# Kernel tuning notes

Measured on AMD Instinct MI355X. Metric: run time of the kernel, lower is better.

The kernel has to match this reference:

```python
import jax, jax.numpy as jnp
import numpy as np

# WikiText-103 adaptive softmax config
CUTOFFS = (0, 20000, 40000, 200000, 267735)  # cluster boundaries


def setup_inputs() -> dict:
    key = jax.random.key(0)
    ks = jax.random.split(key, 12)
    N, D = 1024, 1024
    rn = lambda k, shape, std: jax.random.normal(k, shape, jnp.float32) * std
    return {
        "hidden": jax.random.normal(ks[0], (N, D), jnp.float32),
        "target": jax.random.randint(ks[1], (N,), 0, CUTOFFS[-1], jnp.int32),
        "head_w": rn(ks[2], (20000, 1024), 0.02),
        "head_b": jnp.zeros((20000,), jnp.float32),
        "cluster_w": rn(ks[3], (3, 1024), 0.02),
        "cluster_b": jnp.zeros((3,), jnp.float32),
        "proj0": rn(ks[4], (1024, 1024), 0.01),
        "proj1": rn(ks[5], (1024, 256), 0.01),
        "proj2": rn(ks[6], (1024, 64), 0.01),
        "proj3": rn(ks[7], (1024, 16), 0.01),
        "w1": rn(ks[8], (20000, 256), 0.02),
        "b1": jnp.zeros((20000,), jnp.float32),
        "w2": rn(ks[9], (160000, 64), 0.02),
        "b2": jnp.zeros((160000,), jnp.float32),
        "w3": rn(ks[10], (67735, 16), 0.02),
        "b3": jnp.zeros((67735,), jnp.float32),
    }


def _logit(h, w, b, proj):
    # F.linear(F.linear(h, proj.t()), w, b) == (h @ proj) @ w.T + b
    return (h @ proj) @ w.T + b


def reference(hidden, target, head_w, head_b, cluster_w, cluster_b,
              proj0, proj1, proj2, proj3, w1, b1, w2, b2, w3, b3):
    # head: shortlist vocab (20000) + 3 cluster logits -> [N, 20003]
    hw = jnp.concatenate([head_w, cluster_w], axis=0)
    hb = jnp.concatenate([head_b, cluster_b], axis=0)
    head_lp = jax.nn.log_softmax(_logit(hidden, hw, hb, proj0), axis=-1)

    # cluster 0 (shortlist): logprob directly from head
    t0 = jnp.clip(target, 0, CUTOFFS[1] - 1)
    lp = jnp.take_along_axis(head_lp, t0[:, None].astype(jnp.int32), axis=1)[:, 0]

    tails = [(w1, b1, proj1), (w2, b2, proj2), (w3, b3, proj3)]
    for i, (w, b, p) in enumerate(tails, start=1):
        l, r = CUTOFFS[i], CUTOFFS[i + 1]
        mask = (target >= l) & (target < r)
        ti = jnp.clip(target - l, 0, r - l - 1)
        tail_lp = jax.nn.log_softmax(_logit(hidden, w, b, p), axis=-1)  # [N, r-l]
        # note: torch code indexes head_logprob[:, -i] (reversed cluster order quirk)
        lpi = head_lp[:, -i] + jnp.take_along_axis(tail_lp, ti[:, None], axis=1)[:, 0]
        lp = jnp.where(mask, lpi, lp)

    return -lp  # nll per token, keep_order semantics
```

## Files before the change

kernel.cpp:

```cpp
#include <hip/hip_runtime.h>
#include <math.h>

typedef __bf16 bf16;
typedef __bf16 bf16x4 __attribute__((ext_vector_type(4)));
typedef __bf16 bf16x8 __attribute__((ext_vector_type(8)));
typedef float  f32x4  __attribute__((ext_vector_type(4)));

__device__ __forceinline__ f32x4 mfma16x16x32(bf16x8 a, bf16x8 b, f32x4 c) {
  return __builtin_amdgcn_mfma_f32_16x16x32_bf16(a, b, c, 0, 0, 0);
}

__device__ __forceinline__ void async16(const bf16* gp, bf16* lp) {
  __builtin_amdgcn_global_load_lds(
      (const __attribute__((address_space(1))) void*)gp,
      (__attribute__((address_space(3))) void*)lp, 16, 0, 0);
}

__global__ void __launch_bounds__(256) megaconvert_kernel(
    const float* __restrict__ hidden, const float* __restrict__ head_w,
    const float* __restrict__ cluster_w, const float* __restrict__ w1,
    const float* __restrict__ w2, const float* __restrict__ w3,
    bf16* __restrict__ hid_b, bf16* __restrict__ Wh, bf16* __restrict__ W1b,
    bf16* __restrict__ W2b, bf16* __restrict__ W3b) {
  int b = blockIdx.x;
  const float* in; bf16* out; int n4, tot; int w3mode = 0;
  if (b < 1024)       { in = hidden;    out = hid_b; n4 = 262144;  tot = 262144;  }
  else if (b < 21024) { in = head_w;    out = Wh;    n4 = 5120000; tot = 5120000; b -= 1024; }
  else if (b < 21120) { in = cluster_w; out = Wh + (size_t)20000 * 1024; n4 = 768; tot = 24576; b -= 21024; }
  else if (b < 26144) { in = w1;        out = W1b;   n4 = 1280000; tot = 1286144; b -= 21120; }
  else if (b < 36144) { in = w2;        out = W2b;   n4 = 2560000; tot = 2560000; b -= 26144; }
  else                { in = w3;        out = W3b;   n4 = 270940;  tot = 271360;  b -= 36144; w3mode = 1; }
  int i = b * 256 + threadIdx.x;
  if (i >= tot) return;
  bf16x4 z = {(bf16)0.f, (bf16)0.f, (bf16)0.f, (bf16)0.f};
  bf16x4 v = z;
  if (i < n4) {
    float4 f = ((const float4*)in)[i];
    v = (bf16x4){(bf16)f.x, (bf16)f.y, (bf16)f.z, (bf16)f.w};
  }
  if (!w3mode) {
    ((bf16x4*)out)[i] = v;
  } else {
    int row = i >> 2, kq = i & 3;
    *(bf16x4*)&out[(size_t)row * 32 + kq * 4] = v;
    *(bf16x4*)&out[(size_t)row * 32 + 16 + kq * 4] = z;
  }
}

__global__ void __launch_bounds__(256) transpose_all_kernel(
    const float* __restrict__ proj0, const float* __restrict__ proj1,
    const float* __restrict__ proj2, const float* __restrict__ proj3,
    bf16* __restrict__ Pcat) {
  __shared__ float t[32][33];
  int y = blockIdx.y;
  const float* P; bf16* Pt; int dX, cy;
  if (y < 32)      { P = proj0; Pt = Pcat;                        dX = 1024; cy = y; }
  else if (y < 40) { P = proj1; Pt = Pcat + (size_t)1024 * 1024;  dX = 256;  cy = y - 32; }
  else if (y < 42) { P = proj2; Pt = Pcat + (size_t)1280 * 1024;  dX = 64;   cy = y - 40; }
  else             { P = proj3; Pt = Pcat + (size_t)1344 * 1024;  dX = 16;   cy = y - 42; }
  int tx = threadIdx.x & 31, ty = threadIdx.x >> 5;
  int k0 = blockIdx.x * 32, c0 = cy * 32;
#pragma unroll
  for (int s = 0; s < 4; ++s) {
    int k = k0 + ty + s * 8, col = c0 + tx;
    t[ty + s * 8][tx] = (col < dX) ? P[(size_t)k * dX + col] : 0.f;
  }
  __syncthreads();
#pragma unroll
  for (int s = 0; s < 4; ++s) {
    int colo = c0 + ty + s * 8;
    Pt[(size_t)colo * 1024 + k0 + tx] = (bf16)t[tx][ty + s * 8];
  }
}

__global__ void __launch_bounds__(1024) compact_kernel(const int* __restrict__ target,
                                                       int* __restrict__ rowmap,
                                                       int* __restrict__ slotmap,
                                                       int* __restrict__ counts) {
  __shared__ int cnt[3];
  int tid = threadIdx.x;
  if (tid < 3) cnt[tid] = 0;
  for (int i = tid; i < 3 * 1152; i += 1024) rowmap[i] = 0;
  __syncthreads();
  int t = target[tid];
  int c = (t >= 200000) ? 2 : (t >= 40000) ? 1 : (t >= 20000) ? 0 : -1;
  int slot = -1;
  if (c >= 0) {
    slot = atomicAdd(&cnt[c], 1);
    rowmap[c * 1152 + slot] = tid;
  }
  slotmap[tid] = slot;
  __syncthreads();
  if (tid < 3) counts[tid] = cnt[tid];
}

template <int KDIM, bool LSE>
__global__ void __launch_bounds__(256) gemm_kernel(
    const bf16* __restrict__ A, int strideA,
    const int* __restrict__ rmap, const int* __restrict__ cntp,
    const bf16* __restrict__ B,
    const float* __restrict__ bias, const float* __restrict__ bias2,
    int splice, int V, float* __restrict__ part, int nchunk,
    bf16* __restrict__ Out, int strideOut, int dX) {
  constexpr int BK = 64;
  constexpr int KG = 8;
  constexpr int NIT = KDIM / BK;
  __shared__ bf16 Alds[2][128 * BK];
  __shared__ bf16 Blds[2][128 * BK];
  __shared__ float wpart[2][128];

  const int tid = threadIdx.x;
  const int w = tid >> 6, lane = tid & 63;
  const int q = lane >> 4, c = lane & 15;
  const int wr = w >> 1, wc = w & 1;

  int f = blockIdx.x;
  int xr = f & 7, rb = (f >> 3) & 7, cq = f >> 6;
  int chunk = cq * 8 + xr;
  if (chunk >= nchunk) return;
  const int row0 = rb * 128, col0 = chunk * 128;
  if (cntp && row0 >= *cntp) return;

  int arow[4];
#pragma unroll
  for (int i = 0; i < 4; ++i) {
    int g = i * 256 + tid;
    int r = row0 + (g >> 3);
    arow[i] = rmap ? rmap[r] : r;
  }

  auto stage = [&](int kt, int pb) {
    const int k0 = kt * BK;
#pragma unroll
    for (int i = 0; i < 4; ++i) {
      int g = i * 256 + tid;
      int col = g >> 3, j = g & 7;
      int kg = j ^ (col & 7);
      async16(A + (size_t)arow[i] * strideA + k0 + kg * 8,
              &Alds[pb][(size_t)(g & ~63) * 8]);
      async16(B + (size_t)(col0 + col) * KDIM + k0 + kg * 8,
              &Blds[pb][(size_t)(g & ~63) * 8]);
    }
  };

  f32x4 acc[4][4] = {};

  stage(0, 0);
  for (int kt = 0; kt < NIT; ++kt) {
    const int cb = kt & 1;
    if (kt + 1 < NIT) {
      stage(kt + 1, cb ^ 1);
      asm volatile("s_waitcnt vmcnt(8)" ::: "memory");
    } else {
      asm volatile("s_waitcnt vmcnt(0)" ::: "memory");
    }
    __builtin_amdgcn_sched_barrier(0);
    __builtin_amdgcn_s_barrier();
    asm volatile("" ::: "memory");
    __builtin_amdgcn_s_setprio(1);
#pragma unroll
    for (int ks = 0; ks < BK / 32; ++ks) {
      bf16x8 af[4], bfr[4];
#pragma unroll
      for (int rt = 0; rt < 4; ++rt) {
        int rl = wr * 64 + rt * 16 + c;
        int kq = ks * 4 + q;
        int kg = kq ^ (rl & 7);
        af[rt] = *(const bf16x8*)&Alds[cb][((size_t)rl * KG + kg) * 8];
      }
#pragma unroll
      for (int ct = 0; ct < 4; ++ct) {
        int cl = wc * 64 + ct * 16 + c;
        int kq = ks * 4 + q;
        int kg = kq ^ (cl & 7);
        bfr[ct] = *(const bf16x8*)&Blds[cb][((size_t)cl * KG + kg) * 8];
      }
#pragma unroll
      for (int rt = 0; rt < 4; ++rt)
#pragma unroll
        for (int ct = 0; ct < 4; ++ct)
          acc[rt][ct] = mfma16x16x32(af[rt], bfr[ct], acc[rt][ct]);
    }
    __builtin_amdgcn_s_setprio(0);
    asm volatile("" ::: "memory");
    __builtin_amdgcn_s_barrier();
  }

  if (!LSE) {
#pragma unroll
    for (int rt = 0; rt < 4; ++rt)
#pragma unroll
      for (int ct = 0; ct < 4; ++ct)
#pragma unroll
        for (int r = 0; r < 4; ++r) {
          int col = col0 + wc * 64 + ct * 16 + c;
          if (col < dX) {
            int row = row0 + wr * 64 + rt * 16 + q * 4 + r;
            Out[(size_t)row * strideOut + col] = (bf16)acc[rt][ct][r];
          }
        }
    return;
  }

  float bv[4];
#pragma unroll
  for (int ct = 0; ct < 4; ++ct) {
    int colg = col0 + wc * 64 + ct * 16 + c;
    bv[ct] = (colg < V) ? ((colg < splice) ? bias[colg] : bias2[colg - splice]) : -INFINITY;
  }
#pragma unroll
  for (int rt = 0; rt < 4; ++rt) {
#pragma unroll
    for (int r = 0; r < 4; ++r) {
      float s = 0.f;
#pragma unroll
      for (int ct = 0; ct < 4; ++ct) s += __expf(acc[rt][ct][r] + bv[ct]);
#pragma unroll
      for (int off = 1; off <= 8; off <<= 1) s += __shfl_xor(s, off);
      if (c == 0) wpart[wc][wr * 64 + rt * 16 + q * 4 + r] = s;
    }
  }
  __syncthreads();
  if (tid < 128)
    part[(size_t)chunk * 1024 + row0 + tid] = __logf(wpart[0][tid] + wpart[1][tid]);
}

template <int KDIM, int G>
__global__ void __launch_bounds__(256) gemm_lse_wide_kernel(
    const bf16* __restrict__ A, int strideA,
    const int* __restrict__ rmap, const int* __restrict__ cntp,
    const bf16* __restrict__ B, const float* __restrict__ bias,
    int V, float* __restrict__ part, int nchunk) {
  constexpr int BK = KDIM;
  constexpr int KG = BK / 8;
  constexpr int NL = KG / 2;
  __shared__ bf16 Alds[128 * BK];
  __shared__ bf16 Blds[3][128 * BK];
  __shared__ float biasl[G * 128];
  __shared__ float spart[2][128];

  const int tid = threadIdx.x;
  const int w = tid >> 6, lane = tid & 63;
  const int q = lane >> 4, c = lane & 15;
  const int wr = w >> 1, wc = w & 1;

  const int row0 = blockIdx.y * 128;
  if (row0 >= *cntp) return;
  const int chunk0 = blockIdx.x * G;
  const int nc = (nchunk - chunk0 < G) ? (nchunk - chunk0) : G;

  for (int i = tid; i < G * 128; i += 256) {
    int colg = chunk0 * 128 + i;
    biasl[i] = (colg < V) ? bias[colg] : -INFINITY;
  }
#pragma unroll
  for (int i = 0; i < NL; ++i) {
    int g = i * 256 + tid;
    int row = g / KG, j = g % KG;
    int kg = (KG == 8) ? (j ^ (row & 7)) : (j ^ ((row >> 1) & 3));
    int ar = rmap[row0 + row];
    async16(A + (size_t)ar * strideA + kg * 8, &Alds[(size_t)(g & ~63) * 8]);
  }
#pragma unroll
  for (int b = 0; b < 2; ++b) {
    int ck = (b < nc) ? b : nc - 1;
#pragma unroll
    for (int i = 0; i < NL; ++i) {
      int g = i * 256 + tid;
      int col = g / KG, j = g % KG;
      int kg = (KG == 8) ? (j ^ (col & 7)) : (j ^ ((col >> 1) & 3));
      async16(B + (size_t)((chunk0 + ck) * 128 + col) * KDIM + kg * 8,
              &Blds[b][(size_t)(g & ~63) * 8]);
    }
  }
  __syncthreads();

  bf16x8 af[BK / 32][4];
#pragma unroll
  for (int ks = 0; ks < BK / 32; ++ks)
#pragma unroll
    for (int rt = 0; rt < 4; ++rt) {
      int rl = wr * 64 + rt * 16 + c;
      int kq = ks * 4 + q;
      int kg = (KG == 8) ? (kq ^ (rl & 7)) : (kq ^ ((rl >> 1) & 3));
      af[ks][rt] = *(const bf16x8*)&Alds[((size_t)rl * KG + kg) * 8];
    }

  float sums[4][4] = {};
  int ib = 0;

  for (int ci = 0; ci < nc; ++ci) {
    {
      int pre = (ci + 2 < nc) ? ci + 2 : nc - 1;
      bf16* bw = Blds[(ib == 0) ? 2 : ib - 1];
#pragma unroll
      for (int i = 0; i < NL; ++i) {
        int g = i * 256 + tid;
        int col = g / KG, j = g % KG;
        int kg = (KG == 8) ? (j ^ (col & 7)) : (j ^ ((col >> 1) & 3));
        async16(B + (size_t)((chunk0 + pre) * 128 + col) * KDIM + kg * 8,
                &bw[(size_t)(g & ~63) * 8]);
      }
    }

    const bf16* Bl = Blds[ib];
    f32x4 acc[4][4] = {};
#pragma unroll
    for (int ks = 0; ks < BK / 32; ++ks) {
      bf16x8 bfr[4];
#pragma unroll
      for (int ct = 0; ct < 4; ++ct) {
        int cl = wc * 64 + ct * 16 + c;
        int kq = ks * 4 + q;
        int kg = (KG == 8) ? (kq ^ (cl & 7)) : (kq ^ ((cl >> 1) & 3));
        bfr[ct] = *(const bf16x8*)&Bl[((size_t)cl * KG + kg) * 8];
      }
#pragma unroll
      for (int rt = 0; rt < 4; ++rt)
#pragma unroll
        for (int ct = 0; ct < 4; ++ct)
          acc[rt][ct] = mfma16x16x32(af[ks][rt], bfr[ct], acc[rt][ct]);
    }

    float bv[4];
#pragma unroll
    for (int ct = 0; ct < 4; ++ct) bv[ct] = biasl[ci * 128 + wc * 64 + ct * 16 + c];
#pragma unroll
    for (int rt = 0; rt < 4; ++rt)
#pragma unroll
      for (int r = 0; r < 4; ++r) {
#pragma unroll
        for (int ct = 0; ct < 4; ++ct)
          sums[rt][r] += __expf(acc[rt][ct][r] + bv[ct]);
      }

    if constexpr (NL == 4) asm volatile("s_waitcnt vmcnt(4)" ::: "memory");
    else                   asm volatile("s_waitcnt vmcnt(2)" ::: "memory");
    __builtin_amdgcn_sched_barrier(0);
    __builtin_amdgcn_s_barrier();
    ib = (ib == 2) ? 0 : ib + 1;
  }

#pragma unroll
  for (int rt = 0; rt < 4; ++rt)
#pragma unroll
    for (int r = 0; r < 4; ++r) {
      float s = sums[rt][r];
#pragma unroll
      for (int off = 1; off <= 8; off <<= 1) s += __shfl_xor(s, off);
      if (c == 0) spart[wc][wr * 64 + rt * 16 + q * 4 + r] = s;
    }
  __syncthreads();
  if (tid < 128)
    part[(size_t)blockIdx.x * 1024 + row0 + tid] = __logf(spart[0][tid] + spart[1][tid]);
}

__device__ __forceinline__ float wave_sum64(float v) {
#pragma unroll
  for (int off = 1; off < 64; off <<= 1) v += __shfl_xor(v, off);
  return v;
}
__device__ float lse_cm(const float* __restrict__ p, int n, int idx) {
  int lane = threadIdx.x & 63;
  float s = 0.f;
  for (int i = lane; i < n; i += 64) s += __expf(p[(size_t)i * 1024 + idx]);
  s = wave_sum64(s);
  return __logf(s);
}
__device__ float dot_bw(const bf16* __restrict__ h, const float* __restrict__ wv, int K) {
  int lane = threadIdx.x & 63;
  float s = 0.f;
  for (int i = lane; i < K; i += 64) s += (float)h[i] * wv[i];
  return wave_sum64(s);
}

__global__ void __launch_bounds__(256) final_kernel(
    const int* __restrict__ target, const int* __restrict__ slotmap,
    const float* __restrict__ pH, const float* __restrict__ p1,
    const float* __restrict__ p2, const float* __restrict__ p3,
    const bf16* __restrict__ Hcat,
    const float* __restrict__ head_w, const float* __restrict__ head_b,
    const float* __restrict__ cluster_w, const float* __restrict__ cluster_b,
    const float* __restrict__ w1, const float* __restrict__ b1,
    const float* __restrict__ w2, const float* __restrict__ b2,
    const float* __restrict__ w3, const float* __restrict__ b3,
    float* __restrict__ out) {
  int wv = threadIdx.x >> 6, lane = threadIdx.x & 63;
  int row = blockIdx.x * 4 + wv;
  int t = target[row];
  const bf16* h0 = Hcat + (size_t)row * 1408;

  float lseH = lse_cm(pH, 157, row);
  float lp;
  if (t < 20000) {
    float sel = dot_bw(h0, head_w + (size_t)t * 1024, 1024) + head_b[t];
    lp = sel - lseH;
  } else {
    int i, L, KW, nch, hoff;
    const float* pp; const float* W; const float* Bb;
    if (t < 40000)        { i = 1; L = 20000;  KW = 256; nch = 157; hoff = 1024; pp = p1; W = w1; Bb = b1; }
    else if (t < 200000)  { i = 2; L = 40000;  KW = 64;  nch = 157; hoff = 1280; pp = p2; W = w2; Bb = b2; }
    else                  { i = 3; L = 200000; KW = 16;  nch = 67;  hoff = 1344; pp = p3; W = w3; Bb = b3; }
    int slot = slotmap[row];
    float lseT = lse_cm(pp, nch, slot);
    int ti = t - L;
    float tsel = dot_bw(h0 + hoff, W + (size_t)ti * KW, KW) + Bb[ti];
    int j = 3 - i;
    float csel = dot_bw(h0, cluster_w + (size_t)j * 1024, 1024) + cluster_b[j];
    lp = (csel - lseH) + (tsel - lseT);
  }
  if (lane == 0) out[row] = -lp;
}

extern "C" void kernel_launch(void* const* d_in, const int* in_sizes, int n_in,
                              void* d_out, int out_size, void* d_ws, size_t ws_size,
                              hipStream_t stream) {
  (void)in_sizes; (void)n_in; (void)out_size; (void)ws_size;
  const float* hidden    = (const float*)d_in[0];
  const int*   target    = (const int*)d_in[1];
  const float* head_w    = (const float*)d_in[2];
  const float* head_b    = (const float*)d_in[3];
  const float* cluster_w = (const float*)d_in[4];
  const float* cluster_b = (const float*)d_in[5];
  const float* proj0     = (const float*)d_in[6];
  const float* proj1     = (const float*)d_in[7];
  const float* proj2     = (const float*)d_in[8];
  const float* proj3     = (const float*)d_in[9];
  const float* w1 = (const float*)d_in[10];
  const float* b1 = (const float*)d_in[11];
  const float* w2 = (const float*)d_in[12];
  const float* b2 = (const float*)d_in[13];
  const float* w3 = (const float*)d_in[14];
  const float* b3 = (const float*)d_in[15];
  float* out = (float*)d_out;

  char* p = (char*)d_ws;
  bf16* hid_b = (bf16*)p; p += (size_t)1024 * 1024 * 2;
  bf16* Hcat  = (bf16*)p; p += (size_t)1024 * 1408 * 2;
  bf16* Pcat  = (bf16*)p; p += (size_t)1408 * 1024 * 2;
  bf16* Wh    = (bf16*)p; p += (size_t)20096 * 1024 * 2;
  bf16* W1b   = (bf16*)p; p += (size_t)20096 * 256 * 2;
  bf16* W2b   = (bf16*)p; p += (size_t)160000 * 64 * 2;
  bf16* W3b   = (bf16*)p; p += (size_t)67840 * 32 * 2;
  float* pH   = (float*)p; p += (size_t)157 * 1024 * 4;
  float* p1   = (float*)p; p += (size_t)157 * 1024 * 4;
  float* p2   = (float*)p; p += (size_t)1250 * 1024 * 4;
  float* p3   = (float*)p; p += (size_t)530 * 1024 * 4;
  int* rowmap = (int*)p;  p += 3 * 1152 * 4;
  int* slotmap= (int*)p;  p += 1024 * 4;
  int* counts = (int*)p;  p += 3 * 4;

  compact_kernel<<<1, 1024, 0, stream>>>(target, rowmap, slotmap, counts);

  megaconvert_kernel<<<37204, 256, 0, stream>>>(hidden, head_w, cluster_w, w1, w2, w3,
                                                hid_b, Wh, W1b, W2b, W3b);
  transpose_all_kernel<<<dim3(32, 43), 256, 0, stream>>>(proj0, proj1, proj2, proj3, Pcat);

  gemm_kernel<1024, false><<<128, 256, 0, stream>>>(hid_b, 1024, nullptr, nullptr, Pcat,
                                                    nullptr, nullptr, 0, 0, nullptr, 11,
                                                    Hcat, 1408, 1376);

  gemm_kernel<1024, true><<<64 * 20, 256, 0, stream>>>(Hcat, 1408, nullptr, nullptr, Wh,
                                                       head_b, cluster_b, 20000, 20003,
                                                       pH, 157, nullptr, 0, 0);
  gemm_kernel<256, true><<<64 * 20, 256, 0, stream>>>(Hcat + 1024, 1408, rowmap, counts, W1b,
                                                      b1, b1, 0x40000000, 20000,
                                                      p1, 157, nullptr, 0, 0);

  gemm_lse_wide_kernel<64, 8><<<dim3(157, 8), 256, 0, stream>>>(
      Hcat + 1280, 1408, rowmap + 1152, counts + 1, W2b, b2, 160000, p2, 1250);
  gemm_lse_wide_kernel<32, 8><<<dim3(67, 8), 256, 0, stream>>>(
      Hcat + 1344, 1408, rowmap + 2304, counts + 2, W3b, b3, 67735, p3, 530);

  final_kernel<<<256, 256, 0, stream>>>(target, slotmap, pH, p1, p2, p3, Hcat,
                                        head_w, head_b, cluster_w, cluster_b,
                                        w1, b1, w2, b2, w3, b3, out);
}
```

Before: 382.8 us.

## Replace double-buffered K pipeline with single-stage BK=128 loads per iteration

The GEMM main loop no longer prefetches the next K tile while computing the current one. Each iteration now loads a 128-wide K slab into both LDS halves, synchronizes, computes, and synchronizes again. This halves the iteration count and removes the s_setprio and vmcnt bookkeeping. In exchange it gives up overlap between global loads and MFMA work, so load latency is exposed every iteration.

```diff
diff --git a/kernel.cpp b/kernel.cpp
--- a/kernel.cpp
+++ b/kernel.cpp
@@ -102,11 +102,10 @@
     const float* __restrict__ bias, const float* __restrict__ bias2,
     int splice, int V, float* __restrict__ part, int nchunk,
     bf16* __restrict__ Out, int strideOut, int dX) {
-  constexpr int BK = 64;
-  constexpr int KG = 8;
+  constexpr int BK = 128;
   constexpr int NIT = KDIM / BK;
-  __shared__ bf16 Alds[2][128 * BK];
-  __shared__ bf16 Blds[2][128 * BK];
+  __shared__ bf16 Alds[2][128 * 64];
+  __shared__ bf16 Blds[2][128 * 64];
   __shared__ float wpart[2][128];
 
   const int tid = threadIdx.x;
@@ -129,51 +128,40 @@
     arow[i] = rmap ? rmap[r] : r;
   }
 
-  auto stage = [&](int kt, int pb) {
+  f32x4 acc[4][4] = {};
+
+  for (int kt = 0; kt < NIT; ++kt) {
     const int k0 = kt * BK;
 #pragma unroll
-    for (int i = 0; i < 4; ++i) {
-      int g = i * 256 + tid;
-      int col = g >> 3, j = g & 7;
-      int kg = j ^ (col & 7);
-      async16(A + (size_t)arow[i] * strideA + k0 + kg * 8,
-              &Alds[pb][(size_t)(g & ~63) * 8]);
-      async16(B + (size_t)(col0 + col) * KDIM + k0 + kg * 8,
-              &Blds[pb][(size_t)(g & ~63) * 8]);
-    }
-  };
-
-  f32x4 acc[4][4] = {};
-
-  stage(0, 0);
-  for (int kt = 0; kt < NIT; ++kt) {
-    const int cb = kt & 1;
-    if (kt + 1 < NIT) {
-      stage(kt + 1, cb ^ 1);
-      asm volatile("s_waitcnt vmcnt(8)" ::: "memory");
-    } else {
-      asm volatile("s_waitcnt vmcnt(0)" ::: "memory");
-    }
-    __builtin_amdgcn_sched_barrier(0);
-    __builtin_amdgcn_s_barrier();
-    asm volatile("" ::: "memory");
-    __builtin_amdgcn_s_setprio(1);
-#pragma unroll
-    for (int ks = 0; ks < BK / 32; ++ks) {
+    for (int h = 0; h < 2; ++h)
+#pragma unroll
+      for (int i = 0; i < 4; ++i) {
+        int g = i * 256 + tid;
+        int row = g >> 3, jj = g & 7;
+        int kg = jj ^ (row & 7);
+        async16(A + (size_t)arow[i] * strideA + k0 + h * 64 + kg * 8,
+                &Alds[h][(size_t)(g & ~63) * 8]);
+        async16(B + (size_t)(col0 + row) * KDIM + k0 + h * 64 + kg * 8,
+                &Blds[h][(size_t)(g & ~63) * 8]);
+      }
+    __syncthreads();
+#pragma unroll
+    for (int ks = 0; ks < 4; ++ks) {
+      const bf16* Ah = Alds[ks >> 1];
+      const bf16* Bh = Blds[ks >> 1];
+      const int kqb = (ks & 1) * 4 + q;
       bf16x8 af[4], bfr[4];
 #pragma unroll
       for (int rt = 0; rt < 4; ++rt) {
         int rl = wr * 64 + rt * 16 + c;
-        int kq = ks * 4 + q;
-        int kg = kq ^ (rl & 7);
-        af[rt] = *(const bf16x8*)&Alds[cb][((size_t)rl * KG + kg) * 8];
+        int kg = kqb ^ (rl & 7);
+        af[rt] = *(const bf16x8*)&Ah[((size_t)rl * 8 + kg) * 8];
       }
 #pragma unroll
       for (int ct = 0; ct < 4; ++ct) {
         int cl = wc * 64 + ct * 16 + c;
-        int kq = ks * 4 + q;
-        int kg = kq ^ (cl & 7);
-        bfr[ct] = *(const bf16x8*)&Blds[cb][((size_t)cl * KG + kg) * 8];
+        int kg = kqb ^ (cl & 7);
+        bfr[ct] = *(const bf16x8*)&Bh[((size_t)cl * 8 + kg) * 8];
       }
 #pragma unroll
       for (int rt = 0; rt < 4; ++rt)
@@ -181,9 +169,7 @@
         for (int ct = 0; ct < 4; ++ct)
           acc[rt][ct] = mfma16x16x32(af[rt], bfr[ct], acc[rt][ct]);
     }
-    __builtin_amdgcn_s_setprio(0);
-    asm volatile("" ::: "memory");
-    __builtin_amdgcn_s_barrier();
+    __syncthreads();
   }
 
   if (!LSE) {
```

Measured after the change: 372.3 us. 1.03x faster.
